# Kernel tuning notes

Hardware: AMD Instinct MI355X
Metric: run time of the kernel (lower is better)

The kernel has to match this reference:

```python
import jax, jax.numpy as jnp
import numpy as np

B, N, E, T, F, D, H, HOR = 2, 5000, 40000, 12, 16, 128, 4, 12
C = D // H
NEG_SLOPE = 0.2   # PyG GATConv leaky_relu slope
LN_EPS = 1e-5


def setup_inputs() -> dict:
    key = jax.random.key(0)
    ks = jax.random.split(key, 12)
    s = 0.05
    def rn(k, shape):
        return jax.random.normal(k, shape, jnp.float32) * s
    return {
        "x": jax.random.normal(ks[0], (B, N, T, F), jnp.float32),
        "edge_index": jax.random.randint(ks[1], (2, E), 0, N),
        "edge_weight": jax.random.uniform(ks[2], (E,), dtype=jnp.float32),
        # GATConv params (lin: F->D, att_src/att_dst/att_edge: [H,C], lin_edge: 1->D)
        "W_lin": rn(ks[3], (F, D)),
        "att_src": rn(ks[4], (H, C)),
        "att_dst": rn(ks[5], (H, C)),
        "W_edge": rn(ks[6], (1, D)),
        "att_edge": rn(ks[7], (H, C)),
        "gat_bias": jnp.zeros((D,), jnp.float32),
        # LSTM (1 layer), PyTorch gate order i,f,g,o
        "W_ih": rn(ks[8], (4 * D, D)),
        "W_hh": rn(ks[9], (4 * D, D)),
        "b_ih": jnp.zeros((4 * D,), jnp.float32),
        "b_hh": jnp.zeros((4 * D,), jnp.float32),
        # head: LayerNorm -> Linear(D,D) -> ReLU -> Linear(D,HOR)
        "ln_g": jnp.ones((D,), jnp.float32),
        "ln_b": jnp.zeros((D,), jnp.float32),
        "W1": rn(ks[10], (D, D)),
        "b1": jnp.zeros((D,), jnp.float32),
        "W2": rn(ks[11], (D, HOR)),
        "b2": jnp.zeros((HOR,), jnp.float32),
    }


def _forward(x, edge_weight, W_lin, att_src, att_dst, W_edge, att_edge, gat_bias,
             W_ih, W_hh, b_ih, b_hh, ln_g, ln_b, W1, b1, W2, b2, edge_index):
    b, n, t, f = x.shape
    h, c = att_src.shape
    d = h * c
    src, dst = edge_index[0], edge_index[1]

    # --- GATConv, vectorized over batch and all timesteps at once ---
    hx = jnp.einsum('bntf,fd->bntd', x, W_lin).reshape(b, n, t, h, c)
    a_src = jnp.einsum('bnthc,hc->bnth', hx, att_src)
    a_dst = jnp.einsum('bnthc,hc->bnth', hx, att_dst)
    e_emb = (edge_weight[:, None] * W_edge[0][None, :]).reshape(-1, h, c)  # [E,H,C]
    a_edge = jnp.einsum('ehc,hc->eh', e_emb, att_edge)                     # [E,H]
    alpha = a_src[:, src] + a_dst[:, dst] + a_edge[None, :, None, :]       # [B,E,T,H]
    alpha = jax.nn.leaky_relu(alpha, NEG_SLOPE)
    alpha = jnp.moveaxis(alpha, 1, 0)                                      # [E,B,T,H]
    # scatter-softmax over edges sharing a destination node
    amax = jax.lax.stop_gradient(jax.ops.segment_max(alpha, dst, num_segments=n))
    ex = jnp.exp(alpha - amax[dst])
    den = jax.ops.segment_sum(ex, dst, num_segments=n)
    att = ex / (den[dst] + 1e-16)                                          # [E,B,T,H]
    msg = jnp.moveaxis(hx[:, src], 1, 0) * att[..., None]                  # [E,B,T,H,C]
    agg = jax.ops.segment_sum(msg, dst, num_segments=n)                    # [N,B,T,H,C]
    gnn = jax.nn.elu(jnp.moveaxis(agg, 0, 1).reshape(b, n, t, d) + gat_bias)

    # --- LSTM over time, batch = B*N ---
    rnn_in = gnn.reshape(b * n, t, d)
    def step(carry, xt):
        hh, cc = carry
        g = xt @ W_ih.T + hh @ W_hh.T + b_ih + b_hh
        i, fg, gg, o = jnp.split(g, 4, axis=-1)
        cc = jax.nn.sigmoid(fg) * cc + jax.nn.sigmoid(i) * jnp.tanh(gg)
        hh = jax.nn.sigmoid(o) * jnp.tanh(cc)
        return (hh, cc), None
    z0 = jnp.zeros((b * n, d), x.dtype)
    (hT, _), _ = jax.lax.scan(step, (z0, z0), jnp.moveaxis(rnn_in, 1, 0))

    # --- head: LayerNorm -> Linear -> ReLU -> Linear (dropout = eval/identity) ---
    mu = hT.mean(-1, keepdims=True)
    var = ((hT - mu) ** 2).mean(-1, keepdims=True)
    ln = (hT - mu) / jnp.sqrt(var + LN_EPS) * ln_g + ln_b
    z = jax.nn.relu(ln @ W1 + b1)
    pred = z @ W2 + b2
    return pred.reshape(b, n, -1)


def reference(x, edge_index, edge_weight, W_lin, att_src, att_dst, W_edge, att_edge,
              gat_bias, W_ih, W_hh, b_ih, b_hh, ln_g, ln_b, W1, b1, W2, b2):
    return _forward(x, edge_weight, W_lin, att_src, att_dst, W_edge, att_edge, gat_bias,
                    W_ih, W_hh, b_ih, b_hh, ln_g, ln_b, W1, b1, W2, b2, edge_index)
```

## Files before the change

### kernel.cpp

```cpp
#include <hip/hip_runtime.h>
#include <math.h>

#define BB  2
#define NN  5000
#define EE  40000
#define TT  12
#define FF  16
#define DD  128
#define HH  4
#define HORZ 12
#define NRT (NN * TT)
#define NTILE (NRT / 16)
#define BPB 313

typedef short bf16x8 __attribute__((ext_vector_type(8)));
typedef float f32x4  __attribute__((ext_vector_type(4)));

__device__ __forceinline__ float sigfast(float x) {
    return __fdividef(1.f, 1.f + __expf(-x));
}
__device__ __forceinline__ float tanhfast(float x) {
    return __fdividef(2.f, 1.f + __expf(-2.f * x)) - 1.f;
}

__device__ __forceinline__ unsigned short f2bf(float f) {
    unsigned int u = __float_as_uint(f);
    unsigned int r = (u + 0x7fffu + ((u >> 16) & 1u)) >> 16;
    return (unsigned short)r;
}
__device__ __forceinline__ float bf2f(unsigned short h) {
    return __uint_as_float(((unsigned int)h) << 16);
}

__global__ __launch_bounds__(512) void prep_small(
    const float* __restrict__ W_edge, const float* __restrict__ att_edge,
    const float* __restrict__ b_ih, const float* __restrict__ b_hh,
    float* __restrict__ s_h, float* __restrict__ bias_sum)
{
    int tid = threadIdx.x;
    if (tid < 128) {
        float v = W_edge[tid] * att_edge[tid];
        for (int off = 16; off; off >>= 1) v += __shfl_xor(v, off, 32);
        if ((tid & 31) == 0) s_h[tid >> 5] = v;
    }
    bias_sum[tid] = b_ih[tid] + b_hh[tid];
}

__global__ __launch_bounds__(256) void wfrag_kernel(
    const float* __restrict__ W_ih, const float* __restrict__ W_hh,
    unsigned short* __restrict__ WxF_hi, unsigned short* __restrict__ WxF_lo,
    unsigned short* __restrict__ WhF_hi, unsigned short* __restrict__ WhF_lo)
{
    int gidx = blockIdx.x * 256 + threadIdx.x;
    if (gidx >= 32 * 4 * 64) return;
    int lane = gidx & 63;
    int ks   = (gidx >> 6) & 3;
    int cg   = gidx >> 8;
    int col  = cg * 16 + (lane & 15);
    #pragma unroll
    for (int j = 0; j < 8; ++j) {
        int k = ks * 32 + (lane >> 4) * 8 + j;
        int o = gidx * 8 + j;
        float vx = W_ih[col * DD + k];
        unsigned short xh = f2bf(vx);
        WxF_hi[o] = xh;
        WxF_lo[o] = f2bf(vx - bf2f(xh));
        float vh = W_hh[col * DD + k];
        unsigned short hh = f2bf(vh);
        WhF_hi[o] = hh;
        WhF_lo[o] = f2bf(vh - bf2f(hh));
    }
}

__global__ __launch_bounds__(128) void hx_kernel(
    const float* __restrict__ xb, const float* __restrict__ W_lin,
    const float* __restrict__ att_src, const float* __restrict__ att_dst,
    unsigned short* __restrict__ hxb, float* __restrict__ a_srcT,
    float* __restrict__ a_dstT)
{
    const int rt = blockIdx.x;
    const int d  = threadIdx.x;
    const float* xr = xb + (size_t)rt * FF;
    float acc = 0.f;
    #pragma unroll
    for (int f = 0; f < FF; ++f) acc += xr[f] * W_lin[f * DD + d];
    hxb[(size_t)rt * DD + d] = f2bf(acc);
    float vs = acc * att_src[d];
    float vd = acc * att_dst[d];
    for (int off = 16; off; off >>= 1) {
        vs += __shfl_xor(vs, off, 32);
        vd += __shfl_xor(vd, off, 32);
    }
    if ((d & 31) == 0) {
        int h = d >> 5;
        a_srcT[(size_t)rt * HH + h] = vs;
        a_dstT[(size_t)rt * HH + h] = vd;
    }
}

__global__ __launch_bounds__(256) void count_kernel(const int* __restrict__ dst,
                                                    int* __restrict__ counts)
{
    int e = blockIdx.x * 256 + threadIdx.x;
    if (e < EE) atomicAdd(&counts[dst[e]], 1);
}

__global__ __launch_bounds__(1024) void scan_kernel(const int* __restrict__ counts,
                                                    int* __restrict__ offs,
                                                    int* __restrict__ cur)
{
    __shared__ int part[1024];
    const int tid = threadIdx.x;
    const int CH = 5;
    int base = tid * CH;
    int pre[CH];
    int run = 0;
    #pragma unroll
    for (int i = 0; i < CH; ++i) {
        int idx = base + i;
        int v = (idx < NN) ? counts[idx] : 0;
        pre[i] = run;
        run += v;
    }
    part[tid] = run;
    __syncthreads();
    for (int off = 1; off < 1024; off <<= 1) {
        int v = (tid >= off) ? part[tid - off] : 0;
        __syncthreads();
        part[tid] += v;
        __syncthreads();
    }
    int prefix = (tid == 0) ? 0 : part[tid - 1];
    #pragma unroll
    for (int i = 0; i < CH; ++i) {
        int idx = base + i;
        if (idx < NN) {
            int o = prefix + pre[i];
            offs[idx] = o;
            cur[idx]  = o;
        }
    }
    if (tid == 1023) offs[NN] = part[1023];
}

__global__ __launch_bounds__(256) void fill_kernel(const int* __restrict__ dst,
                                                   int* __restrict__ cur,
                                                   int* __restrict__ elist)
{
    int e = blockIdx.x * 256 + threadIdx.x;
    if (e < EE) {
        int p = atomicAdd(&cur[dst[e]], 1);
        elist[p] = e;
    }
}

__global__ __launch_bounds__(128) void gat_kernel(
    const unsigned short* __restrict__ hxb, const float* __restrict__ a_srcT,
    const float* __restrict__ a_dstT, const int* __restrict__ src_arr,
    const float* __restrict__ ew, const float* __restrict__ s_h,
    const int* __restrict__ offs, const int* __restrict__ elist,
    const float* __restrict__ gat_bias, float* __restrict__ gnn)
{
    const int n = blockIdx.x;
    const int d = threadIdx.x;
    const int h = d >> 5;
    const int e0 = offs[n], e1 = offs[n + 1];
    const float sh = s_h[h];
    const float bias = gat_bias[d];

    const size_t base_dst = (size_t)n * TT;
    float ad[TT];
    #pragma unroll
    for (int t = 0; t < TT; ++t) ad[t] = a_dstT[(base_dst + t) * HH + h];

    float den[TT], acc[TT];
    #pragma unroll
    for (int t = 0; t < TT; ++t) { den[t] = 0.f; acc[t] = 0.f; }

    for (int ii = e0; ii < e1; ++ii) {
        int e = elist[ii];
        int s = src_arr[e];
        float aew = ew[e] * sh;
        const size_t base_src = (size_t)s * TT;
        #pragma unroll
        for (int t = 0; t < TT; ++t) {
            float al = a_srcT[(base_src + t) * HH + h] + ad[t] + aew;
            al = (al >= 0.f) ? al : 0.2f * al;
            float exv = __expf(al);
            den[t] += exv;
            acc[t] += exv * bf2f(hxb[(base_src + t) * DD + d]);
        }
    }
    #pragma unroll
    for (int t = 0; t < TT; ++t) {
        float g = acc[t] / (den[t] + 1e-16f) + bias;
        float o = (g > 0.f) ? g : expm1f(g);
        gnn[((size_t)t * NN + n) * DD + d] = o;
    }
}

__global__ __launch_bounds__(512, 2) void gx_gemm(
    const float* __restrict__ gnn,
    const unsigned short* __restrict__ WxF_hi,
    const unsigned short* __restrict__ WxF_lo,
    const float* __restrict__ bias_s,
    unsigned short* __restrict__ gxS, float* __restrict__ gxG)
{
    __shared__ unsigned short Ahi[64 * 128];
    __shared__ unsigned short Alo[64 * 128];

    const int tid  = threadIdx.x;
    const int wv   = tid >> 6;
    const int lane = tid & 63;
    const int l15  = lane & 15;
    const int g    = lane >> 4;
    const size_t fr0 = (size_t)blockIdx.x * 64;

    #pragma unroll
    for (int c = 0; c < 2; ++c) {
        int linear = tid + c * 512;
        int row = linear >> 4;
        int k0  = (linear & 15) * 8;
        size_t r = fr0 + row;
        if (r > NRT - 1) r = NRT - 1;
        const float* src = gnn + r * DD + k0;
        float4 v0 = *(const float4*)src;
        float4 v1 = *(const float4*)(src + 4);
        float vv[8] = {v0.x, v0.y, v0.z, v0.w, v1.x, v1.y, v1.z, v1.w};
        bf16x8 h8, l8;
        #pragma unroll
        for (int e = 0; e < 8; ++e) {
            unsigned short hb = f2bf(vv[e]);
            h8[e] = (short)hb;
            l8[e] = (short)f2bf(vv[e] - bf2f(hb));
        }
        int byte = (row * 256 + k0 * 2) ^ ((row & 7) << 4);
        *(bf16x8*)((char*)Ahi + byte) = h8;
        *(bf16x8*)((char*)Alo + byte) = l8;
    }

    bf16x8 wh[16], wl[16];
    #pragma unroll
    for (int ct = 0; ct < 4; ++ct)
        #pragma unroll
        for (int ks = 0; ks < 4; ++ks) {
            int fidx = (((wv * 4 + ct) * 4 + ks) * 64 + lane) * 8;
            wh[ct * 4 + ks] = *(const bf16x8*)&WxF_hi[fidx];
            wl[ct * 4 + ks] = *(const bf16x8*)&WxF_lo[fidx];
        }
    #pragma unroll
    for (int i = 0; i < 16; ++i) {
        asm volatile("" : "+v"(wh[i]));
        asm volatile("" : "+v"(wl[i]));
    }
    float bias[4];
    #pragma unroll
    for (int ct = 0; ct < 4; ++ct) bias[ct] = bias_s[(wv * 4 + ct) * 16 + l15];

    __syncthreads();

    #pragma unroll
    for (int ar = 0; ar < 4; ++ar) {
        size_t tile = (size_t)blockIdx.x * 4 + ar;
        if (tile >= NTILE) break;
        bf16x8 ah[4], al[4];
        int row = ar * 16 + l15;
        #pragma unroll
        for (int ks = 0; ks < 4; ++ks) {
            int byte = (row * 256 + (ks * 32 + g * 8) * 2) ^ ((row & 7) << 4);
            ah[ks] = *(const bf16x8*)((const char*)Ahi + byte);
            al[ks] = *(const bf16x8*)((const char*)Alo + byte);
        }
        #pragma unroll
        for (int ct = 0; ct < 4; ++ct) {
            int cg = wv * 4 + ct;
            f32x4 a;
            a[0] = bias[ct]; a[1] = bias[ct]; a[2] = bias[ct]; a[3] = bias[ct];
            #pragma unroll
            for (int ks = 0; ks < 4; ++ks) {
                a = __builtin_amdgcn_mfma_f32_16x16x32_bf16(ah[ks], wh[ct * 4 + ks], a, 0, 0, 0);
                a = __builtin_amdgcn_mfma_f32_16x16x32_bf16(ah[ks], wl[ct * 4 + ks], a, 0, 0, 0);
                a = __builtin_amdgcn_mfma_f32_16x16x32_bf16(al[ks], wh[ct * 4 + ks], a, 0, 0, 0);
            }
            int off = l15 * 16 + g * 4;
            if (cg >= 16 && cg < 24) {
                *(f32x4*)&gxG[(tile * 8 + (cg - 16)) * 256 + off] = a;
            } else {
                int sidx = (cg < 16) ? cg : cg - 8;
                uint2 p;
                p.x = (unsigned)f2bf(a[0]) | ((unsigned)f2bf(a[1]) << 16);
                p.y = (unsigned)f2bf(a[2]) | ((unsigned)f2bf(a[3]) << 16);
                *(uint2*)&gxS[(tile * 24 + sidx) * 256 + off] = p;
            }
        }
    }
}

__global__ __launch_bounds__(512, 2) void lstm_rec(
    const unsigned short* __restrict__ gxS, const float* __restrict__ gxG,
    long sS, long sG,
    const unsigned short* __restrict__ WhF_hi,
    const unsigned short* __restrict__ WhF_lo,
    const float* __restrict__ ln_g, const float* __restrict__ ln_b,
    const float* __restrict__ W1, const float* __restrict__ b1,
    const float* __restrict__ W2, const float* __restrict__ b2,
    float* __restrict__ out)
{
    __shared__ unsigned short hb_hi[2][16 * 128];
    __shared__ unsigned short hb_lo[2][16 * 128];
    __shared__ float lnbuf[16 * 128];
    __shared__ float zbuf[16 * 128];

    const int tid  = threadIdx.x;
    const int wv   = tid >> 6;
    const int lane = tid & 63;
    const int l15  = lane & 15;
    const int g    = lane >> 4;
    const int bat  = blockIdx.x / BPB;
    const int bk   = blockIdx.x - bat * BPB;
    const int r0   = bk * 16;

    gxS += (size_t)bat * sS;
    gxG += (size_t)bat * sG;
    float* outb = out + (size_t)bat * NN * HORZ;

    bf16x8 wh[4][4], wl[4][4];
    #pragma unroll
    for (int gt = 0; gt < 4; ++gt)
        #pragma unroll
        for (int ks = 0; ks < 4; ++ks) {
            int cg = gt * 8 + wv;
            int fidx = ((cg * 4 + ks) * 64 + lane) * 8;
            wh[gt][ks] = *(const bf16x8*)&WhF_hi[fidx];
            wl[gt][ks] = *(const bf16x8*)&WhF_lo[fidx];
        }
    #pragma unroll
    for (int gt = 0; gt < 4; ++gt)
        #pragma unroll
        for (int ks = 0; ks < 4; ++ks) {
            asm volatile("" : "+v"(wh[gt][ks]));
            asm volatile("" : "+v"(wl[gt][ks]));
        }

    int seqq = r0 + g * 4;
    if (seqq > NN - 4) seqq = NN - 4;

    float c4[4] = {0.f, 0.f, 0.f, 0.f};
    f32x4 cin[4], nxt[4];

    {
        size_t F = (size_t)seqq;
        size_t tile = F >> 4;
        int q = ((int)F & 15) >> 2;
        int off = l15 * 16 + q * 4;
        #pragma unroll
        for (int gt = 0; gt < 4; ++gt) {
            if (gt == 2) {
                cin[gt] = *(const f32x4*)&gxG[(tile * 8 + wv) * 256 + off];
            } else {
                int sidx = (gt == 0) ? wv : (gt == 1) ? 8 + wv : 16 + wv;
                uint2 p = *(const uint2*)&gxS[(tile * 24 + sidx) * 256 + off];
                cin[gt][0] = bf2f((unsigned short)(p.x & 0xffff));
                cin[gt][1] = bf2f((unsigned short)(p.x >> 16));
                cin[gt][2] = bf2f((unsigned short)(p.y & 0xffff));
                cin[gt][3] = bf2f((unsigned short)(p.y >> 16));
            }
        }
    }

    for (int t = 0; t < TT; ++t) {
        if (t < TT - 1) {
            size_t F = (size_t)(t + 1) * NN + seqq;
            size_t tile = F >> 4;
            int q = ((int)F & 15) >> 2;
            int off = l15 * 16 + q * 4;
            #pragma unroll
            for (int gt = 0; gt < 4; ++gt) {
                if (gt == 2) {
                    nxt[gt] = *(const f32x4*)&gxG[(tile * 8 + wv) * 256 + off];
                } else {
                    int sidx = (gt == 0) ? wv : (gt == 1) ? 8 + wv : 16 + wv;
                    uint2 p = *(const uint2*)&gxS[(tile * 24 + sidx) * 256 + off];
                    nxt[gt][0] = bf2f((unsigned short)(p.x & 0xffff));
                    nxt[gt][1] = bf2f((unsigned short)(p.x >> 16));
                    nxt[gt][2] = bf2f((unsigned short)(p.y & 0xffff));
                    nxt[gt][3] = bf2f((unsigned short)(p.y >> 16));
                }
            }
        }

        f32x4 acc[4];
        #pragma unroll
        for (int gt = 0; gt < 4; ++gt) acc[gt] = cin[gt];

        if (t > 0) {
            const char* rh = (const char*)hb_hi[t & 1];
            const char* rl = (const char*)hb_lo[t & 1];
            #pragma unroll
            for (int ks = 0; ks < 4; ++ks) {
                int byte = (l15 * 256 + (ks * 32 + g * 8) * 2) ^ ((l15 & 7) << 4);
                bf16x8 ah = *(const bf16x8*)(rh + byte);
                bf16x8 al = *(const bf16x8*)(rl + byte);
                #pragma unroll
                for (int gt = 0; gt < 4; ++gt) {
                    acc[gt] = __builtin_amdgcn_mfma_f32_16x16x32_bf16(ah, wh[gt][ks], acc[gt], 0, 0, 0);
                    acc[gt] = __builtin_amdgcn_mfma_f32_16x16x32_bf16(ah, wl[gt][ks], acc[gt], 0, 0, 0);
                    acc[gt] = __builtin_amdgcn_mfma_f32_16x16x32_bf16(al, wh[gt][ks], acc[gt], 0, 0, 0);
                }
            }
        }

        float hv4[4];
        #pragma unroll
        for (int i = 0; i < 4; ++i) {
            float ig = acc[0][i];
            float fg = acc[1][i];
            float gg = acc[2][i];
            float og = acc[3][i];
            float c = sigfast(fg) * c4[i] + sigfast(ig) * tanhfast(gg);
            c4[i] = c;
            hv4[i] = sigfast(og) * tanhfast(c);
        }

        {
            char* whp = (char*)hb_hi[(t + 1) & 1];
            char* wlp = (char*)hb_lo[(t + 1) & 1];
            #pragma unroll
            for (int i = 0; i < 4; ++i) {
                int row = g * 4 + i;
                int d   = wv * 16 + l15;
                unsigned short hb = f2bf(hv4[i]);
                unsigned short lb = f2bf(hv4[i] - bf2f(hb));
                int byte = (row * 256 + d * 2) ^ ((row & 7) << 4);
                *(unsigned short*)(whp + byte) = hb;
                *(unsigned short*)(wlp + byte) = lb;
            }
        }
        __syncthreads();

        if (t < TT - 1) {
            #pragma unroll
            for (int gt = 0; gt < 4; ++gt) cin[gt] = nxt[gt];
        }
    }

    {
        const int row    = tid >> 5;
        const int lane32 = tid & 31;
        const char* rh = (const char*)hb_hi[0];
        const char* rl = (const char*)hb_lo[0];
        float v[4];
        #pragma unroll
        for (int s = 0; s < 4; ++s) {
            int d = lane32 + s * 32;
            int byte = (row * 256 + d * 2) ^ ((row & 7) << 4);
            v[s] = bf2f(*(const unsigned short*)(rh + byte)) +
                   bf2f(*(const unsigned short*)(rl + byte));
        }
        float sum = v[0] + v[1] + v[2] + v[3];
        for (int off = 16; off; off >>= 1) sum += __shfl_xor(sum, off, 32);
        float mu = sum * (1.f / 128.f);
        float var = 0.f;
        #pragma unroll
        for (int s = 0; s < 4; ++s) { float dv = v[s] - mu; var += dv * dv; }
        for (int off = 16; off; off >>= 1) var += __shfl_xor(var, off, 32);
        float rstd = rsqrtf(var * (1.f / 128.f) + 1e-5f);
        #pragma unroll
        for (int s = 0; s < 4; ++s) {
            int d = lane32 + s * 32;
            lnbuf[row * 128 + d] = (v[s] - mu) * rstd * ln_g[d] + ln_b[d];
        }
    }
    __syncthreads();

    {
        float zv[4];
        #pragma unroll
        for (int s = 0; s < 4; ++s) {
            int lin = tid + s * 512;
            int r2 = lin >> 7, j = lin & 127;
            float a = b1[j];
            #pragma unroll 4
            for (int k = 0; k < 128; ++k) a += lnbuf[r2 * 128 + k] * W1[k * 128 + j];
            zv[s] = fmaxf(a, 0.f);
        }
        #pragma unroll
        for (int s = 0; s < 4; ++s) zbuf[tid + s * 512] = zv[s];
    }
    __syncthreads();

    if (tid < 16 * HORZ) {
        int r2 = tid / HORZ, o = tid % HORZ;
        if (r0 + r2 < NN) {
            float a = b2[o];
            #pragma unroll 4
            for (int k = 0; k < 128; ++k) a += zbuf[r2 * 128 + k] * W2[k * HORZ + o];
            outb[(size_t)(r0 + r2) * HORZ + o] = a;
        }
    }
}

extern "C" void kernel_launch(void* const* d_in, const int* in_sizes, int n_in,
                              void* d_out, int out_size, void* d_ws, size_t ws_size,
                              hipStream_t stream)
{
    const float* x        = (const float*)d_in[0];
    const int*   eidx     = (const int*)d_in[1];
    const float* ew       = (const float*)d_in[2];
    const float* W_lin    = (const float*)d_in[3];
    const float* att_src  = (const float*)d_in[4];
    const float* att_dst  = (const float*)d_in[5];
    const float* W_edge   = (const float*)d_in[6];
    const float* att_edge = (const float*)d_in[7];
    const float* gat_bias = (const float*)d_in[8];
    const float* W_ih     = (const float*)d_in[9];
    const float* W_hh     = (const float*)d_in[10];
    const float* b_ih     = (const float*)d_in[11];
    const float* b_hh     = (const float*)d_in[12];
    const float* ln_g     = (const float*)d_in[13];
    const float* ln_b     = (const float*)d_in[14];
    const float* W1       = (const float*)d_in[15];
    const float* b1       = (const float*)d_in[16];
    const float* W2       = (const float*)d_in[17];
    const float* b2       = (const float*)d_in[18];
    float* out = (float*)d_out;

    char* base = (char*)d_ws;
    float* gnn2            = (float*)base;
    char*  gxb             = base + 30720000;
    unsigned short* gx0S   = (unsigned short*)gxb;
    float*          gx0G   = (float*)(gxb + 46080000);
    unsigned short* gx1S   = (unsigned short*)(gxb + 76800000);
    float*          gx1G   = (float*)(gxb + 76800000 + 46080000);
    char*  tail2           = gxb + 2 * 76800000;
    const long SSTRIDE = 76800000 / 2;
    const long GSTRIDE = 76800000 / 4;

    float* gnn1            = (float*)base;
    float* gxG1            = gnn1 + 7680000;
    unsigned short* gxS1   = (unsigned short*)(gxG1 + 7680000);
    char*  tail1           = (char*)(gxS1 + 23040000);

    size_t tail_bytes = (240000 + 240000 + 512 + 16) * 4 + 4 * 65536 * 2 +
                        (NN + (NN + 8) + NN + EE + 8) * 4;
    size_t need_dual = (size_t)(tail2 - base) + tail_bytes;
    const int dual = (ws_size >= need_dual) ? 1 : 0;

    float* a_srcT  = (float*)(dual ? tail2 : tail1);
    float* a_dstT  = a_srcT + 240000;
    float* bias_s  = a_dstT + 240000;
    float* s_h     = bias_s + 512;
    unsigned short* WxF_hi = (unsigned short*)(s_h + 16);
    unsigned short* WxF_lo = WxF_hi + 65536;
    unsigned short* WhF_hi = WxF_lo + 65536;
    unsigned short* WhF_lo = WhF_hi + 65536;
    int*   counts  = (int*)(WhF_lo + 65536);
    int*   offs    = counts + NN;
    int*   cur     = offs + (NN + 8);
    int*   elist   = cur + NN;

    float* gnn = dual ? gnn2 : gnn1;
    unsigned short* hxb = dual ? gx1S : (unsigned short*)gxG1;

    const int* srcA = eidx;
    const int* dstA = eidx + EE;

    hipMemsetAsync(counts, 0, NN * sizeof(int), stream);
    prep_small<<<1, 512, 0, stream>>>(W_edge, att_edge, b_ih, b_hh, s_h, bias_s);
    wfrag_kernel<<<32, 256, 0, stream>>>(W_ih, W_hh, WxF_hi, WxF_lo, WhF_hi, WhF_lo);
    count_kernel<<<(EE + 255) / 256, 256, 0, stream>>>(dstA, counts);
    scan_kernel<<<1, 1024, 0, stream>>>(counts, offs, cur);
    fill_kernel<<<(EE + 255) / 256, 256, 0, stream>>>(dstA, cur, elist);

    if (dual) {
        for (int b = 0; b < BB; ++b) {
            const float* xb = x + (size_t)b * NN * TT * FF;
            unsigned short* gxSb = b ? gx1S : gx0S;
            float*          gxGb = b ? gx1G : gx0G;
            hx_kernel<<<NRT, 128, 0, stream>>>(xb, W_lin, att_src, att_dst,
                                               hxb, a_srcT, a_dstT);
            gat_kernel<<<NN, 128, 0, stream>>>(hxb, a_srcT, a_dstT, srcA, ew, s_h,
                                               offs, elist, gat_bias, gnn);
            gx_gemm<<<(NRT + 63) / 64, 512, 0, stream>>>(gnn, WxF_hi, WxF_lo,
                                                         bias_s, gxSb, gxGb);
        }
        lstm_rec<<<2 * BPB, 512, 0, stream>>>(gx0S, gx0G, SSTRIDE, GSTRIDE,
                                              WhF_hi, WhF_lo,
                                              ln_g, ln_b, W1, b1, W2, b2, out);
    } else {
        for (int b = 0; b < BB; ++b) {
            const float* xb = x + (size_t)b * NN * TT * FF;
            float* outb = out + (size_t)b * NN * HORZ;
            hx_kernel<<<NRT, 128, 0, stream>>>(xb, W_lin, att_src, att_dst,
                                               hxb, a_srcT, a_dstT);
            gat_kernel<<<NN, 128, 0, stream>>>(hxb, a_srcT, a_dstT, srcA, ew, s_h,
                                               offs, elist, gat_bias, gnn);
            gx_gemm<<<(NRT + 63) / 64, 512, 0, stream>>>(gnn, WxF_hi, WxF_lo,
                                                         bias_s, gxS1, gxG1);
            lstm_rec<<<BPB, 512, 0, stream>>>(gxS1, gxG1, 0, 0,
                                              WhF_hi, WhF_lo,
                                              ln_g, ln_b, W1, b1, W2, b2, outb);
        }
    }
}
```

Baseline: 463.8 us.

## Drop weight low-part MFMAs, widen LSTM tiles, split head into separate kernel

Weights for both the input-projection GEMM and the recurrent LSTM are now kept as a single bf16 part instead of hi/lo pairs, which removes one of the three MFMAs per k-step and halves the weight registers. The LSTM kernel now handles 32 sequences per block in two 16-row tiles, halving the grid and reusing the register-resident weights across more rows. The LayerNorm/MLP head moves out into its own kernel that reads the final hidden state from global memory. The cost is lower weight precision, plus an extra launch and a global round trip for hT.

```diff
diff --git a/kernel.cpp b/kernel.cpp
--- a/kernel.cpp
+++ b/kernel.cpp
@@ -11,7 +11,7 @@
 #define HORZ 12
 #define NRT (NN * TT)
 #define NTILE (NRT / 16)
-#define BPB 313
+#define BPB2 157
 
 typedef short bf16x8 __attribute__((ext_vector_type(8)));
 typedef float f32x4  __attribute__((ext_vector_type(4)));
@@ -48,8 +48,7 @@
 
 __global__ __launch_bounds__(256) void wfrag_kernel(
     const float* __restrict__ W_ih, const float* __restrict__ W_hh,
-    unsigned short* __restrict__ WxF_hi, unsigned short* __restrict__ WxF_lo,
-    unsigned short* __restrict__ WhF_hi, unsigned short* __restrict__ WhF_lo)
+    unsigned short* __restrict__ WxF, unsigned short* __restrict__ WhF)
 {
     int gidx = blockIdx.x * 256 + threadIdx.x;
     if (gidx >= 32 * 4 * 64) return;
@@ -61,14 +60,8 @@
     for (int j = 0; j < 8; ++j) {
         int k = ks * 32 + (lane >> 4) * 8 + j;
         int o = gidx * 8 + j;
-        float vx = W_ih[col * DD + k];
-        unsigned short xh = f2bf(vx);
-        WxF_hi[o] = xh;
-        WxF_lo[o] = f2bf(vx - bf2f(xh));
-        float vh = W_hh[col * DD + k];
-        unsigned short hh = f2bf(vh);
-        WhF_hi[o] = hh;
-        WhF_lo[o] = f2bf(vh - bf2f(hh));
+        WxF[o] = f2bf(W_ih[col * DD + k]);
+        WhF[o] = f2bf(W_hh[col * DD + k]);
     }
 }
 
@@ -201,8 +194,7 @@
 
 __global__ __launch_bounds__(512, 2) void gx_gemm(
     const float* __restrict__ gnn,
-    const unsigned short* __restrict__ WxF_hi,
-    const unsigned short* __restrict__ WxF_lo,
+    const unsigned short* __restrict__ WxF,
     const float* __restrict__ bias_s,
     unsigned short* __restrict__ gxS, float* __restrict__ gxG)
 {
@@ -239,20 +231,16 @@
         *(bf16x8*)((char*)Alo + byte) = l8;
     }
 
-    bf16x8 wh[16], wl[16];
+    bf16x8 wh[16];
     #pragma unroll
     for (int ct = 0; ct < 4; ++ct)
         #pragma unroll
         for (int ks = 0; ks < 4; ++ks) {
             int fidx = (((wv * 4 + ct) * 4 + ks) * 64 + lane) * 8;
-            wh[ct * 4 + ks] = *(const bf16x8*)&WxF_hi[fidx];
-            wl[ct * 4 + ks] = *(const bf16x8*)&WxF_lo[fidx];
-        }
-    #pragma unroll
-    for (int i = 0; i < 16; ++i) {
-        asm volatile("" : "+v"(wh[i]));
-        asm volatile("" : "+v"(wl[i]));
-    }
+            wh[ct * 4 + ks] = *(const bf16x8*)&WxF[fidx];
+        }
+    #pragma unroll
+    for (int i = 0; i < 16; ++i) asm volatile("" : "+v"(wh[i]));
     float bias[4];
     #pragma unroll
     for (int ct = 0; ct < 4; ++ct) bias[ct] = bias_s[(wv * 4 + ct) * 16 + l15];
@@ -279,7 +267,6 @@
             #pragma unroll
             for (int ks = 0; ks < 4; ++ks) {
                 a = __builtin_amdgcn_mfma_f32_16x16x32_bf16(ah[ks], wh[ct * 4 + ks], a, 0, 0, 0);
-                a = __builtin_amdgcn_mfma_f32_16x16x32_bf16(ah[ks], wl[ct * 4 + ks], a, 0, 0, 0);
                 a = __builtin_amdgcn_mfma_f32_16x16x32_bf16(al[ks], wh[ct * 4 + ks], a, 0, 0, 0);
             }
             int off = l15 * 16 + g * 4;
@@ -296,167 +283,160 @@
     }
 }
 
-__global__ __launch_bounds__(512, 2) void lstm_rec(
+__global__ __launch_bounds__(512, 2) void lstm_loop(
     const unsigned short* __restrict__ gxS, const float* __restrict__ gxG,
     long sS, long sG,
-    const unsigned short* __restrict__ WhF_hi,
-    const unsigned short* __restrict__ WhF_lo,
-    const float* __restrict__ ln_g, const float* __restrict__ ln_b,
-    const float* __restrict__ W1, const float* __restrict__ b1,
-    const float* __restrict__ W2, const float* __restrict__ b2,
-    float* __restrict__ out)
-{
-    __shared__ unsigned short hb_hi[2][16 * 128];
-    __shared__ unsigned short hb_lo[2][16 * 128];
-    __shared__ float lnbuf[16 * 128];
-    __shared__ float zbuf[16 * 128];
+    const unsigned short* __restrict__ WhF,
+    float* __restrict__ hT)
+{
+    __shared__ unsigned short hb_hi[2][32 * 128];
+    __shared__ unsigned short hb_lo[2][32 * 128];
 
     const int tid  = threadIdx.x;
     const int wv   = tid >> 6;
     const int lane = tid & 63;
     const int l15  = lane & 15;
     const int g    = lane >> 4;
-    const int bat  = blockIdx.x / BPB;
-    const int bk   = blockIdx.x - bat * BPB;
-    const int r0   = bk * 16;
+    const int bat  = blockIdx.x / BPB2;
+    const int bk   = blockIdx.x - bat * BPB2;
+    const int r0   = bk * 32;
 
     gxS += (size_t)bat * sS;
     gxG += (size_t)bat * sG;
-    float* outb = out + (size_t)bat * NN * HORZ;
-
-    bf16x8 wh[4][4], wl[4][4];
+
+    bf16x8 wh[4][4];
     #pragma unroll
     for (int gt = 0; gt < 4; ++gt)
         #pragma unroll
         for (int ks = 0; ks < 4; ++ks) {
             int cg = gt * 8 + wv;
-            int fidx = ((cg * 4 + ks) * 64 + lane) * 8;
-            wh[gt][ks] = *(const bf16x8*)&WhF_hi[fidx];
-            wl[gt][ks] = *(const bf16x8*)&WhF_lo[fidx];
+            wh[gt][ks] = *(const bf16x8*)&WhF[((cg * 4 + ks) * 64 + lane) * 8];
         }
     #pragma unroll
     for (int gt = 0; gt < 4; ++gt)
         #pragma unroll
-        for (int ks = 0; ks < 4; ++ks) {
-            asm volatile("" : "+v"(wh[gt][ks]));
-            asm volatile("" : "+v"(wl[gt][ks]));
-        }
-
-    int seqq = r0 + g * 4;
-    if (seqq > NN - 4) seqq = NN - 4;
-
-    float c4[4] = {0.f, 0.f, 0.f, 0.f};
-    f32x4 cin[4], nxt[4];
-
-    {
-        size_t F = (size_t)seqq;
+        for (int ks = 0; ks < 4; ++ks) asm volatile("" : "+v"(wh[gt][ks]));
+
+    int seqq[2];
+    #pragma unroll
+    for (int rt = 0; rt < 2; ++rt) {
+        int s = r0 + rt * 16 + g * 4;
+        seqq[rt] = (s > NN - 4) ? (NN - 4) : s;
+    }
+
+    float c8[2][4] = {{0.f,0.f,0.f,0.f},{0.f,0.f,0.f,0.f}};
+    uint2  cS[2][3];  f32x4 cG[2];
+    uint2  nS[2][3];  f32x4 nG[2];
+
+    #pragma unroll
+    for (int rt = 0; rt < 2; ++rt) {
+        size_t F = (size_t)seqq[rt];
         size_t tile = F >> 4;
-        int q = ((int)F & 15) >> 2;
-        int off = l15 * 16 + q * 4;
-        #pragma unroll
-        for (int gt = 0; gt < 4; ++gt) {
-            if (gt == 2) {
-                cin[gt] = *(const f32x4*)&gxG[(tile * 8 + wv) * 256 + off];
-            } else {
-                int sidx = (gt == 0) ? wv : (gt == 1) ? 8 + wv : 16 + wv;
-                uint2 p = *(const uint2*)&gxS[(tile * 24 + sidx) * 256 + off];
-                cin[gt][0] = bf2f((unsigned short)(p.x & 0xffff));
-                cin[gt][1] = bf2f((unsigned short)(p.x >> 16));
-                cin[gt][2] = bf2f((unsigned short)(p.y & 0xffff));
-                cin[gt][3] = bf2f((unsigned short)(p.y >> 16));
-            }
-        }
+        int off = l15 * 16 + (((int)F & 15) >> 2) * 4;
+        cS[rt][0] = *(const uint2*)&gxS[(tile * 24 + wv) * 256 + off];
+        cS[rt][1] = *(const uint2*)&gxS[(tile * 24 + 8 + wv) * 256 + off];
+        cS[rt][2] = *(const uint2*)&gxS[(tile * 24 + 16 + wv) * 256 + off];
+        cG[rt]    = *(const f32x4*)&gxG[(tile * 8 + wv) * 256 + off];
     }
 
     for (int t = 0; t < TT; ++t) {
         if (t < TT - 1) {
-            size_t F = (size_t)(t + 1) * NN + seqq;
-            size_t tile = F >> 4;
-            int q = ((int)F & 15) >> 2;
-            int off = l15 * 16 + q * 4;
             #pragma unroll
-            for (int gt = 0; gt < 4; ++gt) {
-                if (gt == 2) {
-                    nxt[gt] = *(const f32x4*)&gxG[(tile * 8 + wv) * 256 + off];
-                } else {
-                    int sidx = (gt == 0) ? wv : (gt == 1) ? 8 + wv : 16 + wv;
-                    uint2 p = *(const uint2*)&gxS[(tile * 24 + sidx) * 256 + off];
-                    nxt[gt][0] = bf2f((unsigned short)(p.x & 0xffff));
-                    nxt[gt][1] = bf2f((unsigned short)(p.x >> 16));
-                    nxt[gt][2] = bf2f((unsigned short)(p.y & 0xffff));
-                    nxt[gt][3] = bf2f((unsigned short)(p.y >> 16));
+            for (int rt = 0; rt < 2; ++rt) {
+                size_t F = (size_t)(t + 1) * NN + seqq[rt];
+                size_t tile = F >> 4;
+                int off = l15 * 16 + (((int)F & 15) >> 2) * 4;
+                nS[rt][0] = *(const uint2*)&gxS[(tile * 24 + wv) * 256 + off];
+                nS[rt][1] = *(const uint2*)&gxS[(tile * 24 + 8 + wv) * 256 + off];
+                nS[rt][2] = *(const uint2*)&gxS[(tile * 24 + 16 + wv) * 256 + off];
+                nG[rt]    = *(const f32x4*)&gxG[(tile * 8 + wv) * 256 + off];
+            }
+        }
+
+        #pragma unroll
+        for (int rt = 0; rt < 2; ++rt) {
+            f32x4 acc[4];
+            #pragma unroll
+            for (int s = 0; s < 3; ++s) {
+                int gt = (s == 2) ? 3 : s;
+                acc[gt][0] = bf2f((unsigned short)(cS[rt][s].x & 0xffff));
+                acc[gt][1] = bf2f((unsigned short)(cS[rt][s].x >> 16));
+                acc[gt][2] = bf2f((unsigned short)(cS[rt][s].y & 0xffff));
+                acc[gt][3] = bf2f((unsigned short)(cS[rt][s].y >> 16));
+            }
+            acc[2] = cG[rt];
+
+            if (t > 0) {
+                const char* rh = (const char*)hb_hi[t & 1];
+                const char* rl = (const char*)hb_lo[t & 1];
+                #pragma unroll
+                for (int ks = 0; ks < 4; ++ks) {
+                    int row = rt * 16 + l15;
+                    int byte = (row * 256 + (ks * 32 + g * 8) * 2) ^ ((row & 7) << 4);
+                    bf16x8 ah = *(const bf16x8*)(rh + byte);
+                    bf16x8 al = *(const bf16x8*)(rl + byte);
+                    #pragma unroll
+                    for (int gt = 0; gt < 4; ++gt) {
+                        acc[gt] = __builtin_amdgcn_mfma_f32_16x16x32_bf16(ah, wh[gt][ks], acc[gt], 0, 0, 0);
+                        acc[gt] = __builtin_amdgcn_mfma_f32_16x16x32_bf16(al, wh[gt][ks], acc[gt], 0, 0, 0);
+                    }
                 }
             }
-        }
-
-        f32x4 acc[4];
-        #pragma unroll
-        for (int gt = 0; gt < 4; ++gt) acc[gt] = cin[gt];
-
-        if (t > 0) {
-            const char* rh = (const char*)hb_hi[t & 1];
-            const char* rl = (const char*)hb_lo[t & 1];
-            #pragma unroll
-            for (int ks = 0; ks < 4; ++ks) {
-                int byte = (l15 * 256 + (ks * 32 + g * 8) * 2) ^ ((l15 & 7) << 4);
-                bf16x8 ah = *(const bf16x8*)(rh + byte);
-                bf16x8 al = *(const bf16x8*)(rl + byte);
-                #pragma unroll
-                for (int gt = 0; gt < 4; ++gt) {
-                    acc[gt] = __builtin_amdgcn_mfma_f32_16x16x32_bf16(ah, wh[gt][ks], acc[gt], 0, 0, 0);
-                    acc[gt] = __builtin_amdgcn_mfma_f32_16x16x32_bf16(ah, wl[gt][ks], acc[gt], 0, 0, 0);
-                    acc[gt] = __builtin_amdgcn_mfma_f32_16x16x32_bf16(al, wh[gt][ks], acc[gt], 0, 0, 0);
-                }
-            }
-        }
-
-        float hv4[4];
-        #pragma unroll
-        for (int i = 0; i < 4; ++i) {
-            float ig = acc[0][i];
-            float fg = acc[1][i];
-            float gg = acc[2][i];
-            float og = acc[3][i];
-            float c = sigfast(fg) * c4[i] + sigfast(ig) * tanhfast(gg);
-            c4[i] = c;
-            hv4[i] = sigfast(og) * tanhfast(c);
-        }
-
-        {
-            char* whp = (char*)hb_hi[(t + 1) & 1];
-            char* wlp = (char*)hb_lo[(t + 1) & 1];
+
             #pragma unroll
             for (int i = 0; i < 4; ++i) {
-                int row = g * 4 + i;
-                int d   = wv * 16 + l15;
-                unsigned short hb = f2bf(hv4[i]);
-                unsigned short lb = f2bf(hv4[i] - bf2f(hb));
-                int byte = (row * 256 + d * 2) ^ ((row & 7) << 4);
-                *(unsigned short*)(whp + byte) = hb;
-                *(unsigned short*)(wlp + byte) = lb;
-            }
-        }
-        __syncthreads();
+                float c = sigfast(acc[1][i]) * c8[rt][i] +
+                          sigfast(acc[0][i]) * tanhfast(acc[2][i]);
+                c8[rt][i] = c;
+                float hv = sigfast(acc[3][i]) * tanhfast(c);
+                if (t < TT - 1) {
+                    char* whp = (char*)hb_hi[(t + 1) & 1];
+                    char* wlp = (char*)hb_lo[(t + 1) & 1];
+                    int row = rt * 16 + g * 4 + i;
+                    int d   = wv * 16 + l15;
+                    unsigned short hb = f2bf(hv);
+                    int byte = (row * 256 + d * 2) ^ ((row & 7) << 4);
+                    *(unsigned short*)(whp + byte) = hb;
+                    *(unsigned short*)(wlp + byte) = f2bf(hv - bf2f(hb));
+                } else {
+                    int row = r0 + rt * 16 + g * 4 + i;
+                    if (row < NN)
+                        hT[((size_t)bat * NN + row) * DD + wv * 16 + l15] = hv;
+                }
+            }
+        }
 
         if (t < TT - 1) {
+            __syncthreads();
             #pragma unroll
-            for (int gt = 0; gt < 4; ++gt) cin[gt] = nxt[gt];
-        }
-    }
+            for (int rt = 0; rt < 2; ++rt) {
+                cS[rt][0] = nS[rt][0]; cS[rt][1] = nS[rt][1]; cS[rt][2] = nS[rt][2];
+                cG[rt] = nG[rt];
+            }
+        }
+    }
+}
+
+__global__ __launch_bounds__(512, 4) void head_kernel(
+    const float* __restrict__ hT,
+    const float* __restrict__ ln_g, const float* __restrict__ ln_b,
+    const float* __restrict__ W1, const float* __restrict__ b1,
+    const float* __restrict__ W2, const float* __restrict__ b2,
+    float* __restrict__ out, int nrows)
+{
+    __shared__ float lnbuf[16 * 128];
+    __shared__ float zbuf[16 * 128];
+
+    const int tid = threadIdx.x;
+    const int r0  = blockIdx.x * 16;
 
     {
         const int row    = tid >> 5;
         const int lane32 = tid & 31;
-        const char* rh = (const char*)hb_hi[0];
-        const char* rl = (const char*)hb_lo[0];
+        int gr = r0 + row; if (gr > nrows - 1) gr = nrows - 1;
         float v[4];
         #pragma unroll
-        for (int s = 0; s < 4; ++s) {
-            int d = lane32 + s * 32;
-            int byte = (row * 256 + d * 2) ^ ((row & 7) << 4);
-            v[s] = bf2f(*(const unsigned short*)(rh + byte)) +
-                   bf2f(*(const unsigned short*)(rl + byte));
-        }
+        for (int s = 0; s < 4; ++s) v[s] = hT[(size_t)gr * DD + lane32 + s * 32];
         float sum = v[0] + v[1] + v[2] + v[3];
         for (int off = 16; off; off >>= 1) sum += __shfl_xor(sum, off, 32);
         float mu = sum * (1.f / 128.f);
@@ -491,11 +471,11 @@
 
     if (tid < 16 * HORZ) {
         int r2 = tid / HORZ, o = tid % HORZ;
-        if (r0 + r2 < NN) {
+        if (r0 + r2 < nrows) {
             float a = b2[o];
             #pragma unroll 4
             for (int k = 0; k < 128; ++k) a += zbuf[r2 * 128 + k] * W2[k * HORZ + o];
-            outb[(size_t)(r0 + r2) * HORZ + o] = a;
+            out[(size_t)(r0 + r2) * HORZ + o] = a;
         }
     }
 }
@@ -541,7 +521,7 @@
     unsigned short* gxS1   = (unsigned short*)(gxG1 + 7680000);
     char*  tail1           = (char*)(gxS1 + 23040000);
 
-    size_t tail_bytes = (240000 + 240000 + 512 + 16) * 4 + 4 * 65536 * 2 +
+    size_t tail_bytes = (240000 + 240000 + 512 + 16) * 4 + 2 * 65536 * 2 +
                         (NN + (NN + 8) + NN + EE + 8) * 4;
     size_t need_dual = (size_t)(tail2 - base) + tail_bytes;
     const int dual = (ws_size >= need_dual) ? 1 : 0;
@@ -550,16 +530,15 @@
     float* a_dstT  = a_srcT + 240000;
     float* bias_s  = a_dstT + 240000;
     float* s_h     = bias_s + 512;
-    unsigned short* WxF_hi = (unsigned short*)(s_h + 16);
-    unsigned short* WxF_lo = WxF_hi + 65536;
-    unsigned short* WhF_hi = WxF_lo + 65536;
-    unsigned short* WhF_lo = WhF_hi + 65536;
-    int*   counts  = (int*)(WhF_lo + 65536);
+    unsigned short* WxF = (unsigned short*)(s_h + 16);
+    unsigned short* WhF = WxF + 65536;
+    int*   counts  = (int*)(WhF + 65536);
     int*   offs    = counts + NN;
     int*   cur     = offs + (NN + 8);
     int*   elist   = cur + NN;
 
     float* gnn = dual ? gnn2 : gnn1;
+    float* hT  = gnn;
     unsigned short* hxb = dual ? gx1S : (unsigned short*)gxG1;
 
     const int* srcA = eidx;
@@ -567,7 +546,7 @@
 
     hipMemsetAsync(counts, 0, NN * sizeof(int), stream);
     prep_small<<<1, 512, 0, stream>>>(W_edge, att_edge, b_ih, b_hh, s_h, bias_s);
-    wfrag_kernel<<<32, 256, 0, stream>>>(W_ih, W_hh, WxF_hi, WxF_lo, WhF_hi, WhF_lo);
+    wfrag_kernel<<<32, 256, 0, stream>>>(W_ih, W_hh, WxF, WhF);
     count_kernel<<<(EE + 255) / 256, 256, 0, stream>>>(dstA, counts);
     scan_kernel<<<1, 1024, 0, stream>>>(counts, offs, cur);
     fill_kernel<<<(EE + 255) / 256, 256, 0, stream>>>(dstA, cur, elist);
@@ -581,12 +560,14 @@
                                                hxb, a_srcT, a_dstT);
             gat_kernel<<<NN, 128, 0, stream>>>(hxb, a_srcT, a_dstT, srcA, ew, s_h,
                                                offs, elist, gat_bias, gnn);
-            gx_gemm<<<(NRT + 63) / 64, 512, 0, stream>>>(gnn, WxF_hi, WxF_lo,
-                                                         bias_s, gxSb, gxGb);
-        }
-        lstm_rec<<<2 * BPB, 512, 0, stream>>>(gx0S, gx0G, SSTRIDE, GSTRIDE,
-                                              WhF_hi, WhF_lo,
-                                              ln_g, ln_b, W1, b1, W2, b2, out);
+            gx_gemm<<<(NRT + 63) / 64, 512, 0, stream>>>(gnn, WxF, bias_s,
+                                                         gxSb, gxGb);
+        }
+        lstm_loop<<<BB * BPB2, 512, 0, stream>>>(gx0S, gx0G, SSTRIDE, GSTRIDE,
+                                                 WhF, hT);
+        head_kernel<<<(BB * NN) / 16, 512, 0, stream>>>(hT, ln_g, ln_b,
+                                                        W1, b1, W2, b2,
+                                                        out, BB * NN);
     } else {
         for (int b = 0; b < BB; ++b) {
             const float* xb = x + (size_t)b * NN * TT * FF;
@@ -595,11 +576,12 @@
                                                hxb, a_srcT, a_dstT);
             gat_kernel<<<NN, 128, 0, stream>>>(hxb, a_srcT, a_dstT, srcA, ew, s_h,
                                                offs, elist, gat_bias, gnn);
-            gx_gemm<<<(NRT + 63) / 64, 512, 0, stream>>>(gnn, WxF_hi, WxF_lo,
-                                                         bias_s, gxS1, gxG1);
-            lstm_rec<<<BPB, 512, 0, stream>>>(gxS1, gxG1, 0, 0,
-                                              WhF_hi, WhF_lo,
-                                              ln_g, ln_b, W1, b1, W2, b2, outb);
-        }
-    }
-}
+            gx_gemm<<<(NRT + 63) / 64, 512, 0, stream>>>(gnn, WxF, bias_s,
+                                                         gxS1, gxG1);
+            lstm_loop<<<BPB2, 512, 0, stream>>>(gxS1, gxG1, 0, 0, WhF, hT);
+            head_kernel<<<(NN + 15) / 16, 512, 0, stream>>>(hT, ln_g, ln_b,
+                                                            W1, b1, W2, b2,
+                                                            outb, NN);
+        }
+    }
+}
```

After: 427.3 us. 1.09x faster.
